# Kernel tuning notes

Hardware: AMD Instinct MI355X
Metric: run time of the kernel (lower is better)

Reference implementation:

```python
import jax, jax.numpy as jnp
import numpy as np

N = 50000
E = 800000
IN_F, HID, OUT_F = 512, 256, 64
KEEP = 0.5  # Dropout(0.5)


def setup_inputs() -> dict:
    key = jax.random.key(0)
    ks = jax.random.split(key, 7)
    X = jax.random.normal(ks[0], (N, IN_F), dtype=jnp.float32)
    # Xavier-uniform-style init for the two layer weights
    lim1 = float(np.sqrt(6.0 / (IN_F + HID)))
    lim2 = float(np.sqrt(6.0 / (HID + OUT_F)))
    W1 = jax.random.uniform(ks[1], (IN_F, HID), jnp.float32, -lim1, lim1)
    W2 = jax.random.uniform(ks[2], (HID, OUT_F), jnp.float32, -lim2, lim2)
    a_row = jnp.sort(jax.random.randint(ks[3], (E,), 0, N)).astype(jnp.int64)
    a_col = jax.random.randint(ks[4], (E,), 0, N).astype(jnp.int64)
    a_val = jax.random.uniform(ks[5], (E,), jnp.float32)
    drop_mask = jax.random.randint(ks[6], (N, HID), 0, 2).astype(jnp.int32)
    return {"X": X, "W1": W1, "W2": W2, "a_row": a_row, "a_col": a_col,
            "a_val": a_val, "drop_mask": drop_mask}


def _spmm(a_row, a_col, a_val, dense):
    # A @ dense where A is [N, N] sparse in COO form: gather + weighted segment-sum
    msgs = a_val[:, None] * dense[a_col]          # [E, d]
    return jax.ops.segment_sum(msgs, a_row, num_segments=N)


def reference(X, W1, W2, a_row, a_col, a_val, drop_mask):
    # layer 1: feature transform + neighbor aggregation
    h = _spmm(a_row, a_col, a_val, X @ W1)        # [N, HID]
    h = jax.nn.relu(h)
    h = h * drop_mask.astype(h.dtype) * (1.0 / KEEP)  # Dropout(0.5), train mode
    # layer 2
    out = _spmm(a_row, a_col, a_val, h @ W2)      # [N, OUT_F]
    return jax.nn.log_softmax(out, axis=1)
```

## Files before the change

kernel.cpp:

```cpp
#include <hip/hip_runtime.h>
#include <hip/hip_fp16.h>
#include <math.h>

#define NN   50000
#define EE   800000
#define INF  512
#define HIDF 256
#define OUTF 64
#define MTILES (NN/16)

using half8  = __attribute__((ext_vector_type(8))) _Float16;
using half2v = __attribute__((ext_vector_type(2))) _Float16;
using f32x4  = __attribute__((ext_vector_type(4))) float;

#if __has_builtin(__builtin_amdgcn_fdot2)
#define HAS_DOT2 1
#else
#define HAS_DOT2 0
#endif

__global__ void k_prep(const int* __restrict__ a_row, int* __restrict__ row_ptr,
                       const float* __restrict__ W1, _Float16* __restrict__ W1p,
                       const float* __restrict__ W2, _Float16* __restrict__ W2T){
  int b = blockIdx.x, tid = threadIdx.x;
  if (b < 196){
    int i = b * 256 + tid;
    if (i > NN) return;
    int lo = 0, hi = EE;
    while (lo < hi){ int mid = (lo + hi) >> 1; if (a_row[mid] < i) lo = mid + 1; else hi = mid; }
    row_ptr[i] = lo;
  } else if (b < 708){
    int idx = (b - 196) * 256 + tid;
    int k = idx >> 8, col = idx & 255;
    int kk = k >> 5, k2 = k & 31;
    W1p[((kk << 8) + col) * 32 + k2] = (_Float16)W1[idx];
  } else {
    int idx = (b - 708) * 256 + tid;
    int k = idx >> 6, n = idx & 63;
    W2T[n * HIDF + k] = (_Float16)W2[idx];
  }
}

__global__ __launch_bounds__(128) void k_gemm1(const float* __restrict__ X,
                                               const _Float16* __restrict__ W1p,
                                               _Float16* __restrict__ XW1s){
  int wave = threadIdx.x >> 6, lane = threadIdx.x & 63;
  int l16 = lane & 15, quad = lane >> 4;
  int m0 = blockIdx.x * 64 + wave * 32;
  int r0 = min(m0 + l16, NN - 1);
  int r1 = min(m0 + 16 + l16, NN - 1);
  const float* arow0 = X + (size_t)r0 * INF + quad * 8;
  const float* arow1 = X + (size_t)r1 * INF + quad * 8;

  f32x4 acc0[16], acc1[16];
  #pragma unroll
  for (int t = 0; t < 16; t++){ acc0[t] = (f32x4){0.f,0.f,0.f,0.f}; acc1[t] = (f32x4){0.f,0.f,0.f,0.f}; }

  for (int kk = 0; kk < INF/32; kk++){
    const float4* ap0 = (const float4*)(arow0 + kk * 32);
    const float4* ap1 = (const float4*)(arow1 + kk * 32);
    float4 a00 = ap0[0], a01 = ap0[1];
    float4 a10 = ap1[0], a11 = ap1[1];
    half8 af0, af1;
    af0[0]=(_Float16)a00.x; af0[1]=(_Float16)a00.y; af0[2]=(_Float16)a00.z; af0[3]=(_Float16)a00.w;
    af0[4]=(_Float16)a01.x; af0[5]=(_Float16)a01.y; af0[6]=(_Float16)a01.z; af0[7]=(_Float16)a01.w;
    af1[0]=(_Float16)a10.x; af1[1]=(_Float16)a10.y; af1[2]=(_Float16)a10.z; af1[3]=(_Float16)a10.w;
    af1[4]=(_Float16)a11.x; af1[5]=(_Float16)a11.y; af1[6]=(_Float16)a11.z; af1[7]=(_Float16)a11.w;

    const _Float16* bchunk = W1p + kk * (256*32);
    #pragma unroll
    for (int nt = 0; nt < 16; nt++){
      half8 bf = *(const half8*)(bchunk + (nt*16 + l16) * 32 + quad * 8);
      acc0[nt] = __builtin_amdgcn_mfma_f32_16x16x32_f16(af0, bf, acc0[nt], 0, 0, 0);
      acc1[nt] = __builtin_amdgcn_mfma_f32_16x16x32_f16(af1, bf, acc1[nt], 0, 0, 0);
    }
  }
  #pragma unroll
  for (int nt = 0; nt < 16; nt++){
    int s = nt >> 1;
    _Float16* base = XW1s + (size_t)s * NN * 32 + (nt & 1) * 16 + l16;
    #pragma unroll
    for (int r = 0; r < 4; r++){
      int row0 = m0 + quad*4 + r;
      int row1 = m0 + 16 + quad*4 + r;
      if (row0 < NN) base[(size_t)row0 * 32] = (_Float16)acc0[nt][r];
      if (row1 < NN) base[(size_t)row1 * 32] = (_Float16)acc1[nt][r];
    }
  }
}

__global__ __launch_bounds__(256) void k_spmm1(const int* __restrict__ row_ptr,
                                               const int* __restrict__ a_col,
                                               const float* __restrict__ a_val,
                                               const _Float16* __restrict__ XW1s,
                                               const int* __restrict__ drop_mask,
                                               _Float16* __restrict__ hb){
  int s  = blockIdx.x & 7;
  int rg = blockIdx.x >> 3;
  int wave = threadIdx.x >> 6, lane = threadIdx.x & 63;
  int row_local = lane >> 4;
  int grp = (lane >> 2) & 3;
  int q   = lane & 3;
  int r = rg * 16 + wave * 4 + row_local;
  int es = row_ptr[r], ee = row_ptr[r+1];
  const _Float16* Xs = XW1s + (size_t)s * NN * 32 + q * 8;

  float acc[8] = {0,0,0,0,0,0,0,0};
  int i = es + grp;
  for (; i + 4 < ee; i += 8){
    float v0 = a_val[i];     int c0 = a_col[i];
    float v1 = a_val[i+4];   int c1 = a_col[i+4];
    int4 x0 = *(const int4*)(Xs + (size_t)c0 * 32);
    int4 x1 = *(const int4*)(Xs + (size_t)c1 * 32);
#if HAS_DOT2
    half2v vv = { (_Float16)v0, (_Float16)v1 };
    const int xs0[4] = {x0.x, x0.y, x0.z, x0.w};
    const int xs1[4] = {x1.x, x1.y, x1.z, x1.w};
    #pragma unroll
    for (int d = 0; d < 4; d++){
      int lo = __builtin_amdgcn_perm(xs1[d], xs0[d], 0x05040100);
      int hi = __builtin_amdgcn_perm(xs1[d], xs0[d], 0x07060302);
      acc[2*d]   = __builtin_amdgcn_fdot2(__builtin_bit_cast(half2v, lo), vv, acc[2*d],   false);
      acc[2*d+1] = __builtin_amdgcn_fdot2(__builtin_bit_cast(half2v, hi), vv, acc[2*d+1], false);
    }
#else
    const int xs0[4] = {x0.x, x0.y, x0.z, x0.w};
    const int xs1[4] = {x1.x, x1.y, x1.z, x1.w};
    #pragma unroll
    for (int d = 0; d < 4; d++){
      half2v h0 = __builtin_bit_cast(half2v, xs0[d]);
      half2v h1 = __builtin_bit_cast(half2v, xs1[d]);
      acc[2*d]   += v0 * (float)h0.x + v1 * (float)h1.x;
      acc[2*d+1] += v0 * (float)h0.y + v1 * (float)h1.y;
    }
#endif
  }
  for (; i < ee; i += 4){
    float v = a_val[i];  int c = a_col[i];
    int4 x = *(const int4*)(Xs + (size_t)c * 32);
    const int xs[4] = {x.x, x.y, x.z, x.w};
    #pragma unroll
    for (int d = 0; d < 4; d++){
      half2v h = __builtin_bit_cast(half2v, xs[d]);
      acc[2*d]   += v * (float)h.x;
      acc[2*d+1] += v * (float)h.y;
    }
  }
  #pragma unroll
  for (int j = 0; j < 8; j++){
    acc[j] += __shfl_xor(acc[j], 4);
    acc[j] += __shfl_xor(acc[j], 8);
  }
  if (grp == 0){
    const int* dm = drop_mask + (size_t)r * HIDF + s * 32 + q * 8;
    int4 d0 = *(const int4*)(dm);
    int4 d1 = *(const int4*)(dm + 4);
    half8 o;
    o[0] = (_Float16)(fmaxf(acc[0],0.f) * (float)d0.x * 2.0f);
    o[1] = (_Float16)(fmaxf(acc[1],0.f) * (float)d0.y * 2.0f);
    o[2] = (_Float16)(fmaxf(acc[2],0.f) * (float)d0.z * 2.0f);
    o[3] = (_Float16)(fmaxf(acc[3],0.f) * (float)d0.w * 2.0f);
    o[4] = (_Float16)(fmaxf(acc[4],0.f) * (float)d1.x * 2.0f);
    o[5] = (_Float16)(fmaxf(acc[5],0.f) * (float)d1.y * 2.0f);
    o[6] = (_Float16)(fmaxf(acc[6],0.f) * (float)d1.z * 2.0f);
    o[7] = (_Float16)(fmaxf(acc[7],0.f) * (float)d1.w * 2.0f);
    *(half8*)(hb + (size_t)r * HIDF + s * 32 + q * 8) = o;
  }
}

__global__ __launch_bounds__(256) void k_gemm2(const _Float16* __restrict__ A,
                                               const _Float16* __restrict__ BT,
                                               _Float16* __restrict__ HW2s){
  int wave = threadIdx.x >> 6, lane = threadIdx.x & 63;
  int tile_m = blockIdx.x * 4 + wave;
  if (tile_m >= MTILES) return;
  int m0 = tile_m * 16, l16 = lane & 15, quad = lane >> 4;

  f32x4 acc[4];
  #pragma unroll
  for (int t = 0; t < 4; t++) acc[t] = (f32x4){0.f,0.f,0.f,0.f};

  const _Float16* ar = A + (size_t)(m0 + l16) * HIDF + quad * 8;
  for (int kk = 0; kk < HIDF/32; kk++){
    half8 af = *(const half8*)(ar + kk * 32);
    #pragma unroll
    for (int nt = 0; nt < 4; nt++){
      half8 bf = *(const half8*)(BT + (size_t)(nt*16 + l16) * HIDF + kk*32 + quad*8);
      acc[nt] = __builtin_amdgcn_mfma_f32_16x16x32_f16(af, bf, acc[nt], 0, 0, 0);
    }
  }
  #pragma unroll
  for (int nt = 0; nt < 4; nt++){
    _Float16* base = HW2s + (size_t)nt * NN * 16 + l16;
    #pragma unroll
    for (int r = 0; r < 4; r++)
      base[(size_t)(m0 + quad*4 + r) * 16] = (_Float16)acc[nt][r];
  }
}

__global__ __launch_bounds__(256) void k_spmm2(const int* __restrict__ row_ptr,
                                               const int* __restrict__ a_col,
                                               const float* __restrict__ a_val,
                                               const _Float16* __restrict__ HW2s,
                                               float* __restrict__ out){
  int t  = blockIdx.x & 3;
  int rg = blockIdx.x >> 2;
  int wave = threadIdx.x >> 6, lane = threadIdx.x & 63;
  int row_local = lane >> 4;
  int grp = (lane >> 2) & 3;
  int q   = lane & 3;
  int r = rg * 16 + wave * 4 + row_local;
  int es = row_ptr[r], ee = row_ptr[r+1];
  const _Float16* Hs = HW2s + (size_t)t * NN * 16 + q * 4;

  float acc[4] = {0,0,0,0};
  int i = es + grp;
  for (; i + 4 < ee; i += 8){
    float v0 = a_val[i];     int c0 = a_col[i];
    float v1 = a_val[i+4];   int c1 = a_col[i+4];
    int2 x0 = *(const int2*)(Hs + (size_t)c0 * 16);
    int2 x1 = *(const int2*)(Hs + (size_t)c1 * 16);
#if HAS_DOT2
    half2v vv = { (_Float16)v0, (_Float16)v1 };
    const int xs0[2] = {x0.x, x0.y};
    const int xs1[2] = {x1.x, x1.y};
    #pragma unroll
    for (int d = 0; d < 2; d++){
      int lo = __builtin_amdgcn_perm(xs1[d], xs0[d], 0x05040100);
      int hi = __builtin_amdgcn_perm(xs1[d], xs0[d], 0x07060302);
      acc[2*d]   = __builtin_amdgcn_fdot2(__builtin_bit_cast(half2v, lo), vv, acc[2*d],   false);
      acc[2*d+1] = __builtin_amdgcn_fdot2(__builtin_bit_cast(half2v, hi), vv, acc[2*d+1], false);
    }
#else
    const int xs0[2] = {x0.x, x0.y};
    const int xs1[2] = {x1.x, x1.y};
    #pragma unroll
    for (int d = 0; d < 2; d++){
      half2v h0 = __builtin_bit_cast(half2v, xs0[d]);
      half2v h1 = __builtin_bit_cast(half2v, xs1[d]);
      acc[2*d]   += v0 * (float)h0.x + v1 * (float)h1.x;
      acc[2*d+1] += v0 * (float)h0.y + v1 * (float)h1.y;
    }
#endif
  }
  for (; i < ee; i += 4){
    float v = a_val[i];  int c = a_col[i];
    int2 x = *(const int2*)(Hs + (size_t)c * 16);
    const int xs[2] = {x.x, x.y};
    #pragma unroll
    for (int d = 0; d < 2; d++){
      half2v h = __builtin_bit_cast(half2v, xs[d]);
      acc[2*d]   += v * (float)h.x;
      acc[2*d+1] += v * (float)h.y;
    }
  }
  #pragma unroll
  for (int j = 0; j < 4; j++){
    acc[j] += __shfl_xor(acc[j], 4);
    acc[j] += __shfl_xor(acc[j], 8);
  }
  if (grp == 0){
    float4 o4 = { acc[0], acc[1], acc[2], acc[3] };
    *(float4*)(out + (size_t)r * OUTF + t * 16 + q * 4) = o4;
  }
}

__global__ __launch_bounds__(256) void k_lsm(float* __restrict__ out){
  int wave = threadIdx.x >> 6, lane = threadIdx.x & 63;
  int r = blockIdx.x * 4 + wave;
  float x = out[(size_t)r * OUTF + lane];
  float m = x;
  #pragma unroll
  for (int o = 1; o <= 32; o <<= 1) m = fmaxf(m, __shfl_xor(m, o));
  float ssum = expf(x - m);
  #pragma unroll
  for (int o = 1; o <= 32; o <<= 1) ssum += __shfl_xor(ssum, o);
  out[(size_t)r * OUTF + lane] = x - m - logf(ssum);
}

extern "C" void kernel_launch(void* const* d_in, const int* in_sizes, int n_in,
                              void* d_out, int out_size, void* d_ws, size_t ws_size,
                              hipStream_t stream) {
  const float* X      = (const float*)d_in[0];
  const float* W1     = (const float*)d_in[1];
  const float* W2     = (const float*)d_in[2];
  const int*   a_row  = (const int*)d_in[3];
  const int*   a_col  = (const int*)d_in[4];
  const float* a_val  = (const float*)d_in[5];
  const int*   drop   = (const int*)d_in[6];
  float*       out    = (float*)d_out;

  char* ws = (char*)d_ws;
  int*       row_ptr = (int*)      (ws);
  _Float16*  W1p     = (_Float16*)(ws + 200704);
  _Float16*  W2T     = (_Float16*)(ws + 462848);
  _Float16*  XW1s    = (_Float16*)(ws + 495616);
  _Float16*  hb      = (_Float16*)(ws + 26095616);
  _Float16*  HW2s    = (_Float16*)(ws + 51695616);

  k_prep<<<772, 256, 0, stream>>>(a_row, row_ptr, W1, W1p, W2, W2T);
  k_gemm1<<<(NN + 63)/64, 128, 0, stream>>>(X, W1p, XW1s);
  k_spmm1<<<8 * (NN/16), 256, 0, stream>>>(row_ptr, a_col, a_val, XW1s, drop, hb);
  k_gemm2<<<(MTILES + 3)/4, 256, 0, stream>>>(hb, W2T, HW2s);
  k_spmm2<<<4 * (NN/16), 256, 0, stream>>>(row_ptr, a_col, a_val, HW2s, out);
  k_lsm<<<NN/4, 256, 0, stream>>>(out);
}
```

Before: 392.1 us.

## Fuse layer-2 SpMM with log-softmax and retile first GEMM per wave

The second SpMM now keeps the full 64-wide output row in one wave, reading a row-major HW2 instead of a 4-way column-sliced layout, and applies log-softmax in registers before writing. This removes the separate log-softmax kernel and its re-read and re-write of the output. k_gemm1 now gives each wave a single 16-row tile instead of two, with 256-thread blocks and an occupancy hint, trading B-fragment reuse for lower register pressure and more waves in flight.

Result: faster. 368.7 us (-6.0%).

```diff
diff --git a/kernel.cpp b/kernel.cpp
--- a/kernel.cpp
+++ b/kernel.cpp
@@ -41,38 +41,32 @@
   }
 }
 
-__global__ __launch_bounds__(128) void k_gemm1(const float* __restrict__ X,
-                                               const _Float16* __restrict__ W1p,
-                                               _Float16* __restrict__ XW1s){
+__global__ __launch_bounds__(256, 4) void k_gemm1(const float* __restrict__ X,
+                                                  const _Float16* __restrict__ W1p,
+                                                  _Float16* __restrict__ XW1s){
   int wave = threadIdx.x >> 6, lane = threadIdx.x & 63;
   int l16 = lane & 15, quad = lane >> 4;
-  int m0 = blockIdx.x * 64 + wave * 32;
-  int r0 = min(m0 + l16, NN - 1);
-  int r1 = min(m0 + 16 + l16, NN - 1);
-  const float* arow0 = X + (size_t)r0 * INF + quad * 8;
-  const float* arow1 = X + (size_t)r1 * INF + quad * 8;
-
-  f32x4 acc0[16], acc1[16];
-  #pragma unroll
-  for (int t = 0; t < 16; t++){ acc0[t] = (f32x4){0.f,0.f,0.f,0.f}; acc1[t] = (f32x4){0.f,0.f,0.f,0.f}; }
+  int tile = blockIdx.x * 4 + wave;
+  if (tile >= MTILES) return;
+  int m0 = tile * 16;
+  const float* arow = X + (size_t)(m0 + l16) * INF + quad * 8;
+
+  f32x4 acc[16];
+  #pragma unroll
+  for (int t = 0; t < 16; t++) acc[t] = (f32x4){0.f,0.f,0.f,0.f};
 
   for (int kk = 0; kk < INF/32; kk++){
-    const float4* ap0 = (const float4*)(arow0 + kk * 32);
-    const float4* ap1 = (const float4*)(arow1 + kk * 32);
-    float4 a00 = ap0[0], a01 = ap0[1];
-    float4 a10 = ap1[0], a11 = ap1[1];
-    half8 af0, af1;
-    af0[0]=(_Float16)a00.x; af0[1]=(_Float16)a00.y; af0[2]=(_Float16)a00.z; af0[3]=(_Float16)a00.w;
-    af0[4]=(_Float16)a01.x; af0[5]=(_Float16)a01.y; af0[6]=(_Float16)a01.z; af0[7]=(_Float16)a01.w;
-    af1[0]=(_Float16)a10.x; af1[1]=(_Float16)a10.y; af1[2]=(_Float16)a10.z; af1[3]=(_Float16)a10.w;
-    af1[4]=(_Float16)a11.x; af1[5]=(_Float16)a11.y; af1[6]=(_Float16)a11.z; af1[7]=(_Float16)a11.w;
+    const float4* ap = (const float4*)(arow + kk * 32);
+    float4 a0 = ap[0], a1 = ap[1];
+    half8 af;
+    af[0]=(_Float16)a0.x; af[1]=(_Float16)a0.y; af[2]=(_Float16)a0.z; af[3]=(_Float16)a0.w;
+    af[4]=(_Float16)a1.x; af[5]=(_Float16)a1.y; af[6]=(_Float16)a1.z; af[7]=(_Float16)a1.w;
 
     const _Float16* bchunk = W1p + kk * (256*32);
     #pragma unroll
     for (int nt = 0; nt < 16; nt++){
       half8 bf = *(const half8*)(bchunk + (nt*16 + l16) * 32 + quad * 8);
-      acc0[nt] = __builtin_amdgcn_mfma_f32_16x16x32_f16(af0, bf, acc0[nt], 0, 0, 0);
-      acc1[nt] = __builtin_amdgcn_mfma_f32_16x16x32_f16(af1, bf, acc1[nt], 0, 0, 0);
+      acc[nt] = __builtin_amdgcn_mfma_f32_16x16x32_f16(af, bf, acc[nt], 0, 0, 0);
     }
   }
   #pragma unroll
@@ -80,12 +74,8 @@
     int s = nt >> 1;
     _Float16* base = XW1s + (size_t)s * NN * 32 + (nt & 1) * 16 + l16;
     #pragma unroll
-    for (int r = 0; r < 4; r++){
-      int row0 = m0 + quad*4 + r;
-      int row1 = m0 + 16 + quad*4 + r;
-      if (row0 < NN) base[(size_t)row0 * 32] = (_Float16)acc0[nt][r];
-      if (row1 < NN) base[(size_t)row1 * 32] = (_Float16)acc1[nt][r];
-    }
+    for (int r = 0; r < 4; r++)
+      base[(size_t)(m0 + quad*4 + r) * 32] = (_Float16)acc[nt][r];
   }
 }
 
@@ -170,7 +160,7 @@
 
 __global__ __launch_bounds__(256) void k_gemm2(const _Float16* __restrict__ A,
                                                const _Float16* __restrict__ BT,
-                                               _Float16* __restrict__ HW2s){
+                                               _Float16* __restrict__ HW2){
   int wave = threadIdx.x >> 6, lane = threadIdx.x & 63;
   int tile_m = blockIdx.x * 4 + wave;
   if (tile_m >= MTILES) return;
@@ -191,51 +181,47 @@
   }
   #pragma unroll
   for (int nt = 0; nt < 4; nt++){
-    _Float16* base = HW2s + (size_t)nt * NN * 16 + l16;
+    int col = nt*16 + l16;
     #pragma unroll
     for (int r = 0; r < 4; r++)
-      base[(size_t)(m0 + quad*4 + r) * 16] = (_Float16)acc[nt][r];
-  }
-}
-
-__global__ __launch_bounds__(256) void k_spmm2(const int* __restrict__ row_ptr,
-                                               const int* __restrict__ a_col,
-                                               const float* __restrict__ a_val,
-                                               const _Float16* __restrict__ HW2s,
-                                               float* __restrict__ out){
-  int t  = blockIdx.x & 3;
-  int rg = blockIdx.x >> 2;
-  int wave = threadIdx.x >> 6, lane = threadIdx.x & 63;
-  int row_local = lane >> 4;
-  int grp = (lane >> 2) & 3;
-  int q   = lane & 3;
-  int r = rg * 16 + wave * 4 + row_local;
-  int es = row_ptr[r], ee = row_ptr[r+1];
-  const _Float16* Hs = HW2s + (size_t)t * NN * 16 + q * 4;
-
-  float acc[4] = {0,0,0,0};
-  int i = es + grp;
-  for (; i + 4 < ee; i += 8){
+      HW2[(size_t)(m0 + quad*4 + r) * OUTF + col] = (_Float16)acc[nt][r];
+  }
+}
+
+__global__ __launch_bounds__(256) void k_spmm2_lsm(const int* __restrict__ row_ptr,
+                                                   const int* __restrict__ a_col,
+                                                   const float* __restrict__ a_val,
+                                                   const _Float16* __restrict__ HW2,
+                                                   float* __restrict__ out){
+  int wave = threadIdx.x >> 6, lane = threadIdx.x & 63;
+  int r = blockIdx.x * 4 + wave;
+  int s = row_ptr[r], e = row_ptr[r+1];
+  int g = lane >> 3;
+  int q = lane & 7;
+  float acc[8] = {0,0,0,0,0,0,0,0};
+
+  int i = s + g;
+  for (; i + 8 < e; i += 16){
     float v0 = a_val[i];     int c0 = a_col[i];
-    float v1 = a_val[i+4];   int c1 = a_col[i+4];
-    int2 x0 = *(const int2*)(Hs + (size_t)c0 * 16);
-    int2 x1 = *(const int2*)(Hs + (size_t)c1 * 16);
+    float v1 = a_val[i+8];   int c1 = a_col[i+8];
+    int4 x0 = *(const int4*)(HW2 + (size_t)c0 * OUTF + q * 8);
+    int4 x1 = *(const int4*)(HW2 + (size_t)c1 * OUTF + q * 8);
 #if HAS_DOT2
     half2v vv = { (_Float16)v0, (_Float16)v1 };
-    const int xs0[2] = {x0.x, x0.y};
-    const int xs1[2] = {x1.x, x1.y};
-    #pragma unroll
-    for (int d = 0; d < 2; d++){
+    const int xs0[4] = {x0.x, x0.y, x0.z, x0.w};
+    const int xs1[4] = {x1.x, x1.y, x1.z, x1.w};
+    #pragma unroll
+    for (int d = 0; d < 4; d++){
       int lo = __builtin_amdgcn_perm(xs1[d], xs0[d], 0x05040100);
       int hi = __builtin_amdgcn_perm(xs1[d], xs0[d], 0x07060302);
       acc[2*d]   = __builtin_amdgcn_fdot2(__builtin_bit_cast(half2v, lo), vv, acc[2*d],   false);
       acc[2*d+1] = __builtin_amdgcn_fdot2(__builtin_bit_cast(half2v, hi), vv, acc[2*d+1], false);
     }
 #else
-    const int xs0[2] = {x0.x, x0.y};
-    const int xs1[2] = {x1.x, x1.y};
-    #pragma unroll
-    for (int d = 0; d < 2; d++){
+    const int xs0[4] = {x0.x, x0.y, x0.z, x0.w};
+    const int xs1[4] = {x1.x, x1.y, x1.z, x1.w};
+    #pragma unroll
+    for (int d = 0; d < 4; d++){
       half2v h0 = __builtin_bit_cast(half2v, xs0[d]);
       half2v h1 = __builtin_bit_cast(half2v, xs1[d]);
       acc[2*d]   += v0 * (float)h0.x + v1 * (float)h1.x;
@@ -243,39 +229,41 @@
     }
 #endif
   }
-  for (; i < ee; i += 4){
+  for (; i < e; i += 8){
     float v = a_val[i];  int c = a_col[i];
-    int2 x = *(const int2*)(Hs + (size_t)c * 16);
-    const int xs[2] = {x.x, x.y};
-    #pragma unroll
-    for (int d = 0; d < 2; d++){
+    int4 x = *(const int4*)(HW2 + (size_t)c * OUTF + q * 8);
+    const int xs[4] = {x.x, x.y, x.z, x.w};
+    #pragma unroll
+    for (int d = 0; d < 4; d++){
       half2v h = __builtin_bit_cast(half2v, xs[d]);
       acc[2*d]   += v * (float)h.x;
       acc[2*d+1] += v * (float)h.y;
     }
   }
   #pragma unroll
-  for (int j = 0; j < 4; j++){
-    acc[j] += __shfl_xor(acc[j], 4);
+  for (int j = 0; j < 8; j++){
     acc[j] += __shfl_xor(acc[j], 8);
-  }
-  if (grp == 0){
-    float4 o4 = { acc[0], acc[1], acc[2], acc[3] };
-    *(float4*)(out + (size_t)r * OUTF + t * 16 + q * 4) = o4;
-  }
-}
-
-__global__ __launch_bounds__(256) void k_lsm(float* __restrict__ out){
-  int wave = threadIdx.x >> 6, lane = threadIdx.x & 63;
-  int r = blockIdx.x * 4 + wave;
-  float x = out[(size_t)r * OUTF + lane];
-  float m = x;
-  #pragma unroll
-  for (int o = 1; o <= 32; o <<= 1) m = fmaxf(m, __shfl_xor(m, o));
-  float ssum = expf(x - m);
-  #pragma unroll
-  for (int o = 1; o <= 32; o <<= 1) ssum += __shfl_xor(ssum, o);
-  out[(size_t)r * OUTF + lane] = x - m - logf(ssum);
+    acc[j] += __shfl_xor(acc[j], 16);
+    acc[j] += __shfl_xor(acc[j], 32);
+  }
+  float m = acc[0];
+  #pragma unroll
+  for (int j = 1; j < 8; j++) m = fmaxf(m, acc[j]);
+  #pragma unroll
+  for (int o = 1; o <= 4; o <<= 1) m = fmaxf(m, __shfl_xor(m, o));
+  float ssum = 0.f;
+  #pragma unroll
+  for (int j = 0; j < 8; j++) ssum += expf(acc[j] - m);
+  #pragma unroll
+  for (int o = 1; o <= 4; o <<= 1) ssum += __shfl_xor(ssum, o);
+  float ls = m + logf(ssum);
+  if (g == 0){
+    float4 o0 = { acc[0]-ls, acc[1]-ls, acc[2]-ls, acc[3]-ls };
+    float4 o1 = { acc[4]-ls, acc[5]-ls, acc[6]-ls, acc[7]-ls };
+    float* op = out + (size_t)r * OUTF + q * 8;
+    *(float4*)(op)     = o0;
+    *(float4*)(op + 4) = o1;
+  }
 }
 
 extern "C" void kernel_launch(void* const* d_in, const int* in_sizes, int n_in,
@@ -296,12 +284,11 @@
   _Float16*  W2T     = (_Float16*)(ws + 462848);
   _Float16*  XW1s    = (_Float16*)(ws + 495616);
   _Float16*  hb      = (_Float16*)(ws + 26095616);
-  _Float16*  HW2s    = (_Float16*)(ws + 51695616);
+  _Float16*  HW2     = (_Float16*)(ws + 51695616);
 
   k_prep<<<772, 256, 0, stream>>>(a_row, row_ptr, W1, W1p, W2, W2T);
-  k_gemm1<<<(NN + 63)/64, 128, 0, stream>>>(X, W1p, XW1s);
+  k_gemm1<<<(MTILES + 3)/4, 256, 0, stream>>>(X, W1p, XW1s);
   k_spmm1<<<8 * (NN/16), 256, 0, stream>>>(row_ptr, a_col, a_val, XW1s, drop, hb);
-  k_gemm2<<<(MTILES + 3)/4, 256, 0, stream>>>(hb, W2T, HW2s);
-  k_spmm2<<<4 * (NN/16), 256, 0, stream>>>(row_ptr, a_col, a_val, HW2s, out);
-  k_lsm<<<NN/4, 256, 0, stream>>>(out);
-}
+  k_gemm2<<<(MTILES + 3)/4, 256, 0, stream>>>(hb, W2T, HW2);
+  k_spmm2_lsm<<<NN/4, 256, 0, stream>>>(row_ptr, a_col, a_val, HW2, out);
+}
```
